# Optimization experiments

Measured on AMD Instinct MI355X. Metric: run time of the kernel, lower is better.

Reference implementation:

```python
import jax, jax.numpy as jnp
import numpy as np

B, C = 32, 32768
ENC_DIM, VOCAB, TOK_DIM, HIDDEN = 1024, 100000, 256, 512


def setup_inputs() -> dict:
    key = jax.random.key(0)
    k1, k2, k3, k4, k5 = jax.random.split(key, 5)
    enc_vec = jax.random.normal(k1, (B, ENC_DIM), dtype=jnp.float32)
    cand_tok = jax.random.randint(k2, (B, C), 0, VOCAB, dtype=jnp.int64)
    tok_emb = jax.random.normal(k3, (VOCAB, TOK_DIM), dtype=jnp.float32) * 0.02
    # PAD (0) and BOS (1) rows fixed to zeros, as in __init__
    tok_emb = tok_emb.at[0].set(0.0).at[1].set(0.0)
    W1 = jax.random.normal(k4, (HIDDEN, ENC_DIM), dtype=jnp.float32) * 0.02
    b1 = jnp.zeros((HIDDEN,), dtype=jnp.float32)
    W2 = jax.random.normal(k5, (TOK_DIM, HIDDEN), dtype=jnp.float32) * 0.02
    return {"enc_vec": enc_vec, "cand_tok": cand_tok, "tok_emb": tok_emb,
            "W1": W1, "b1": b1, "W2": W2}


def reference(enc_vec, cand_tok, tok_emb, W1, b1, W2):
    # q_proj: Linear -> GELU (exact, torch default) -> (Dropout inactive at eval) -> Linear (no bias)
    h = jax.nn.gelu(enc_vec @ W1.T + b1, approximate=False)  # (B, hidden)
    q = h @ W2.T                                             # (B, tok_dim)
    Wc = tok_emb[cand_tok]                                   # (B, C, tok_dim) gather
    logits = jnp.einsum('be,bce->bc', q, Wc)                 # (B, C)
    return logits
```

## Files before the change

### kernel.cpp

```cpp
#include <hip/hip_runtime.h>
#include <hip/hip_bf16.h>
#include <math.h>

#define B_    32
#define C_    32768
#define ENC_  1024
#define VOCAB_ 100000
#define TOK_  256
#define HID_  512
#define TILES_ (VOCAB_ / 32)

typedef __attribute__((ext_vector_type(8))) short short8;
typedef __attribute__((ext_vector_type(4))) float f32x4;

__device__ __forceinline__ float gelu_exact(float x) {
    return 0.5f * x * (1.0f + erff(x * 0.70710678118654752f));
}

__device__ __forceinline__ unsigned short f2bf(float f) {
    unsigned u = __builtin_bit_cast(unsigned, f);
    return (unsigned short)((u + 0x7fffu + ((u >> 16) & 1u)) >> 16);
}

__device__ __forceinline__ short8 pack8(float4 a, float4 b) {
    short8 r;
    r[0] = (short)f2bf(a.x); r[1] = (short)f2bf(a.y);
    r[2] = (short)f2bf(a.z); r[3] = (short)f2bf(a.w);
    r[4] = (short)f2bf(b.x); r[5] = (short)f2bf(b.y);
    r[6] = (short)f2bf(b.z); r[7] = (short)f2bf(b.w);
    return r;
}

__global__ __launch_bounds__(256) void k1_hidden(
    const float* __restrict__ enc, const float* __restrict__ W1,
    const float* __restrict__ b1, float* __restrict__ h)
{
    __shared__ float enc_lds[ENC_];
    const int b = blockIdx.y;
    const int tid = threadIdx.x;
    ((float4*)enc_lds)[tid] = ((const float4*)(enc + b * ENC_))[tid];
    __syncthreads();

    const int hw = tid >> 5, lane = tid & 31;
    const int jbase = blockIdx.x * 64 + hw * 8;
    const float4* enc4 = (const float4*)enc_lds;
    #pragma unroll
    for (int i = 0; i < 8; ++i) {
        const int j = jbase + i;
        const float4* wrow = (const float4*)(W1 + (size_t)j * ENC_);
        float acc = 0.f;
        #pragma unroll
        for (int t = 0; t < 8; ++t) {
            const int k4 = t * 32 + lane;
            float4 w = wrow[k4];
            float4 e = enc4[k4];
            acc += w.x * e.x + w.y * e.y + w.z * e.z + w.w * e.w;
        }
        #pragma unroll
        for (int m = 16; m >= 1; m >>= 1) acc += __shfl_xor(acc, m, 32);
        if (lane == 0) h[b * HID_ + j] = gelu_exact(acc + b1[j]);
    }
}

__global__ __launch_bounds__(256) void k2_q(
    const float* __restrict__ h, const float* __restrict__ W2,
    float* __restrict__ q)
{
    __shared__ float h_lds[HID_];
    const int b = blockIdx.y;
    const int tid = threadIdx.x;
    ((float2*)h_lds)[tid] = ((const float2*)(h + b * HID_))[tid];
    __syncthreads();

    const int hw = tid >> 5, lane = tid & 31;
    const int jbase = blockIdx.x * 64 + hw * 8;
    const float4* h4 = (const float4*)h_lds;
    #pragma unroll
    for (int i = 0; i < 8; ++i) {
        const int j = jbase + i;
        const float4* wrow = (const float4*)(W2 + (size_t)j * HID_);
        float acc = 0.f;
        #pragma unroll
        for (int t = 0; t < 4; ++t) {
            const int k4 = t * 32 + lane;
            float4 w = wrow[k4];
            float4 e = h4[k4];
            acc += w.x * e.x + w.y * e.y + w.z * e.z + w.w * e.w;
        }
        #pragma unroll
        for (int m = 16; m >= 1; m >>= 1) acc += __shfl_xor(acc, m, 32);
        if (lane == 0) q[b * TOK_ + j] = acc;
    }
}

__global__ __launch_bounds__(256) void k3_qall_mfma(
    const float* __restrict__ q, const float* __restrict__ tok_emb,
    __hip_bfloat16* __restrict__ q_all, int* __restrict__ counter)
{
    __shared__ short8 q_lds[1024];
    const int tid  = threadIdx.x;
    const int lane = tid & 63;
    const int hw   = tid >> 6;
    const int m  = lane & 15;
    const int kq = lane >> 4;

    #pragma unroll
    for (int ks2 = 0; ks2 < 2; ++ks2) {
        const int ks = hw * 2 + ks2;
        #pragma unroll
        for (int n = 0; n < 2; ++n) {
            const float4* p = (const float4*)(q + (n * 16 + m) * TOK_ + ks * 32 + kq * 8);
            q_lds[(ks * 2 + n) * 64 + lane] = pack8(p[0], p[1]);
        }
    }
    __syncthreads();

    for (;;) {
        int tile;
        if (lane == 0) tile = atomicAdd(counter, 1);
        tile = __builtin_amdgcn_readfirstlane(tile);
        if (tile >= TILES_) break;
        const int v0 = tile * 32;

        const float* abase = tok_emb + (size_t)(v0 + m) * TOK_ + kq * 8;

        float4 st[2][4];
        #pragma unroll
        for (int t = 0; t < 2; ++t) {
            st[0][t * 2 + 0] = *(const float4*)(abase + t * 16 * TOK_);
            st[0][t * 2 + 1] = *(const float4*)(abase + t * 16 * TOK_ + 4);
        }

        f32x4 acc[2][2] = {{{0.f,0.f,0.f,0.f},{0.f,0.f,0.f,0.f}},
                           {{0.f,0.f,0.f,0.f},{0.f,0.f,0.f,0.f}}};
        #pragma unroll
        for (int ks = 0; ks < 8; ++ks) {
            const int cur = ks & 1, nxt = cur ^ 1;
            if (ks < 7) {
                #pragma unroll
                for (int t = 0; t < 2; ++t) {
                    st[nxt][t * 2 + 0] = *(const float4*)(abase + t * 16 * TOK_ + (ks + 1) * 32);
                    st[nxt][t * 2 + 1] = *(const float4*)(abase + t * 16 * TOK_ + (ks + 1) * 32 + 4);
                }
            }
            short8 b0 = q_lds[(ks * 2 + 0) * 64 + lane];
            short8 b1 = q_lds[(ks * 2 + 1) * 64 + lane];
            #pragma unroll
            for (int t = 0; t < 2; ++t) {
                short8 af = pack8(st[cur][t * 2 + 0], st[cur][t * 2 + 1]);
                acc[t][0] = __builtin_amdgcn_mfma_f32_16x16x32_bf16(af, b0, acc[t][0], 0, 0, 0);
                acc[t][1] = __builtin_amdgcn_mfma_f32_16x16x32_bf16(af, b1, acc[t][1], 0, 0, 0);
            }
        }

        #pragma unroll
        for (int t = 0; t < 2; ++t) {
            #pragma unroll
            for (int n = 0; n < 2; ++n) {
                ushort4 r;
                r.x = f2bf(acc[t][n][0]); r.y = f2bf(acc[t][n][1]);
                r.z = f2bf(acc[t][n][2]); r.w = f2bf(acc[t][n][3]);
                __hip_bfloat16* dst = q_all + (size_t)(n * 16 + m) * VOCAB_ + v0 + t * 16 + kq * 4;
                *(ushort4*)dst = r;
            }
        }
    }
}

__global__ __launch_bounds__(256) void k4_gather(
    const int* __restrict__ cand, const __hip_bfloat16* __restrict__ q_all,
    float* __restrict__ out)
{
    const int b     = blockIdx.x & 31;
    const int chunk = blockIdx.x >> 5;
    const int c0 = chunk * 1024 + threadIdx.x * 4;
    const int4 t = *(const int4*)(cand + (size_t)b * C_ + c0);
    const __hip_bfloat16* row = q_all + (size_t)b * VOCAB_;
    float4 r;
    r.x = __bfloat162float(row[t.x]);
    r.y = __bfloat162float(row[t.y]);
    r.z = __bfloat162float(row[t.z]);
    r.w = __bfloat162float(row[t.w]);
    *(float4*)(out + (size_t)b * C_ + c0) = r;
}

extern "C" void kernel_launch(void* const* d_in, const int* in_sizes, int n_in,
                              void* d_out, int out_size, void* d_ws, size_t ws_size,
                              hipStream_t stream) {
    const float* enc     = (const float*)d_in[0];
    const int*   cand    = (const int*)  d_in[1];
    const float* tok_emb = (const float*)d_in[2];
    const float* W1      = (const float*)d_in[3];
    const float* b1      = (const float*)d_in[4];
    const float* W2      = (const float*)d_in[5];
    float* out = (float*)d_out;

    float* h = (float*)d_ws;
    float* q = h + B_ * HID_;
    __hip_bfloat16* q_all = (__hip_bfloat16*)(q + B_ * TOK_);
    int* counter = (int*)((char*)(q_all + (size_t)B_ * VOCAB_) + 256);

    hipMemsetAsync(counter, 0, sizeof(int), stream);

    k1_hidden<<<dim3(8, 32), 256, 0, stream>>>(enc, W1, b1, h);
    k2_q     <<<dim3(4, 32), 256, 0, stream>>>(h, W2, q);
    k3_qall_mfma<<<512, 256, 0, stream>>>(q, tok_emb, q_all, counter);
    k4_gather<<<32 * 32, 256, 0, stream>>>(cand, q_all, out);
}
```

Baseline: 230.2 us.

## Replace atomic work-stealing in k3 with static one-tile-per-wave grid

The persistent k3 kernel, which pulled 32-row vocab tiles from an atomic counter, is replaced by a static launch where each wave handles one 16-row tile, with about 1563 blocks. All eight K-slices of tok_emb are loaded up front instead of double-buffered, and the counter memset launch is dropped. This removes atomic serialization and one launch, and gives the GPU many more waves to hide memory latency. In exchange each block reloads q into LDS, adding redundant LDS staging, and each wave holds more registers for the loads.

```diff
diff --git a/kernel.cpp b/kernel.cpp
--- a/kernel.cpp
+++ b/kernel.cpp
@@ -8,7 +8,7 @@
 #define VOCAB_ 100000
 #define TOK_  256
 #define HID_  512
-#define TILES_ (VOCAB_ / 32)
+#define HTILES_ (VOCAB_ / 16)
 
 typedef __attribute__((ext_vector_type(8))) short short8;
 typedef __attribute__((ext_vector_type(4))) float f32x4;
@@ -95,7 +95,7 @@
 
 __global__ __launch_bounds__(256) void k3_qall_mfma(
     const float* __restrict__ q, const float* __restrict__ tok_emb,
-    __hip_bfloat16* __restrict__ q_all, int* __restrict__ counter)
+    __hip_bfloat16* __restrict__ q_all)
 {
     __shared__ short8 q_lds[1024];
     const int tid  = threadIdx.x;
@@ -115,56 +115,35 @@
     }
     __syncthreads();
 
-    for (;;) {
-        int tile;
-        if (lane == 0) tile = atomicAdd(counter, 1);
-        tile = __builtin_amdgcn_readfirstlane(tile);
-        if (tile >= TILES_) break;
-        const int v0 = tile * 32;
+    const int wave = blockIdx.x * 4 + hw;
+    if (wave >= HTILES_) return;
+    const int v0 = wave * 16;
 
-        const float* abase = tok_emb + (size_t)(v0 + m) * TOK_ + kq * 8;
+    const float* abase = tok_emb + (size_t)(v0 + m) * TOK_ + kq * 8;
 
-        float4 st[2][4];
-        #pragma unroll
-        for (int t = 0; t < 2; ++t) {
-            st[0][t * 2 + 0] = *(const float4*)(abase + t * 16 * TOK_);
-            st[0][t * 2 + 1] = *(const float4*)(abase + t * 16 * TOK_ + 4);
-        }
+    float4 st[16];
+    #pragma unroll
+    for (int ks = 0; ks < 8; ++ks) {
+        st[ks * 2 + 0] = *(const float4*)(abase + ks * 32);
+        st[ks * 2 + 1] = *(const float4*)(abase + ks * 32 + 4);
+    }
 
-        f32x4 acc[2][2] = {{{0.f,0.f,0.f,0.f},{0.f,0.f,0.f,0.f}},
-                           {{0.f,0.f,0.f,0.f},{0.f,0.f,0.f,0.f}}};
-        #pragma unroll
-        for (int ks = 0; ks < 8; ++ks) {
-            const int cur = ks & 1, nxt = cur ^ 1;
-            if (ks < 7) {
-                #pragma unroll
-                for (int t = 0; t < 2; ++t) {
-                    st[nxt][t * 2 + 0] = *(const float4*)(abase + t * 16 * TOK_ + (ks + 1) * 32);
-                    st[nxt][t * 2 + 1] = *(const float4*)(abase + t * 16 * TOK_ + (ks + 1) * 32 + 4);
-                }
-            }
-            short8 b0 = q_lds[(ks * 2 + 0) * 64 + lane];
-            short8 b1 = q_lds[(ks * 2 + 1) * 64 + lane];
-            #pragma unroll
-            for (int t = 0; t < 2; ++t) {
-                short8 af = pack8(st[cur][t * 2 + 0], st[cur][t * 2 + 1]);
-                acc[t][0] = __builtin_amdgcn_mfma_f32_16x16x32_bf16(af, b0, acc[t][0], 0, 0, 0);
-                acc[t][1] = __builtin_amdgcn_mfma_f32_16x16x32_bf16(af, b1, acc[t][1], 0, 0, 0);
-            }
-        }
+    f32x4 acc0 = {0.f, 0.f, 0.f, 0.f};
+    f32x4 acc1 = {0.f, 0.f, 0.f, 0.f};
+    #pragma unroll
+    for (int ks = 0; ks < 8; ++ks) {
+        short8 af = pack8(st[ks * 2], st[ks * 2 + 1]);
+        short8 b0 = q_lds[(ks * 2 + 0) * 64 + lane];
+        short8 b1 = q_lds[(ks * 2 + 1) * 64 + lane];
+        acc0 = __builtin_amdgcn_mfma_f32_16x16x32_bf16(af, b0, acc0, 0, 0, 0);
+        acc1 = __builtin_amdgcn_mfma_f32_16x16x32_bf16(af, b1, acc1, 0, 0, 0);
+    }
 
-        #pragma unroll
-        for (int t = 0; t < 2; ++t) {
-            #pragma unroll
-            for (int n = 0; n < 2; ++n) {
-                ushort4 r;
-                r.x = f2bf(acc[t][n][0]); r.y = f2bf(acc[t][n][1]);
-                r.z = f2bf(acc[t][n][2]); r.w = f2bf(acc[t][n][3]);
-                __hip_bfloat16* dst = q_all + (size_t)(n * 16 + m) * VOCAB_ + v0 + t * 16 + kq * 4;
-                *(ushort4*)dst = r;
-            }
-        }
-    }
+    ushort4 r0, r1;
+    r0.x = f2bf(acc0[0]); r0.y = f2bf(acc0[1]); r0.z = f2bf(acc0[2]); r0.w = f2bf(acc0[3]);
+    r1.x = f2bf(acc1[0]); r1.y = f2bf(acc1[1]); r1.z = f2bf(acc1[2]); r1.w = f2bf(acc1[3]);
+    *(ushort4*)(q_all + (size_t)(m)      * VOCAB_ + v0 + kq * 4) = r0;
+    *(ushort4*)(q_all + (size_t)(16 + m) * VOCAB_ + v0 + kq * 4) = r1;
 }
 
 __global__ __launch_bounds__(256) void k4_gather(
@@ -198,12 +177,12 @@
     float* h = (float*)d_ws;
     float* q = h + B_ * HID_;
     __hip_bfloat16* q_all = (__hip_bfloat16*)(q + B_ * TOK_);
-    int* counter = (int*)((char*)(q_all + (size_t)B_ * VOCAB_) + 256);
-
-    hipMemsetAsync(counter, 0, sizeof(int), stream);
 
     k1_hidden<<<dim3(8, 32), 256, 0, stream>>>(enc, W1, b1, h);
     k2_q     <<<dim3(4, 32), 256, 0, stream>>>(h, W2, q);
-    k3_qall_mfma<<<512, 256, 0, stream>>>(q, tok_emb, q_all, counter);
+
+    const int blocks3 = (HTILES_ + 3) / 4;
+    k3_qall_mfma<<<blocks3, 256, 0, stream>>>(q, tok_emb, q_all);
+
     k4_gather<<<32 * 32, 256, 0, stream>>>(cand, q_all, out);
 }
```

After: 192.1 us. 16.6% less time.
